# Kernel tuning notes

Measured on AMD Instinct MI355X. Metric: run time of the kernel, lower is better.

The kernel has to match this reference:

```python
import jax, jax.numpy as jnp
import numpy as np
import math

B, T, D = 4, 2048, 1024
N, D_OUT = 1024, 1024
EPS_A = 1e-4
PROJ_BOUND = 1.0


def setup_inputs() -> dict:
    key = jax.random.key(0)
    ks = jax.random.split(key, 4)
    # reset_parameters: rho=0.99, delta0=1.0
    rho, delta0 = 0.99, 1.0
    alpha0 = -math.log(rho) / delta0
    alpha_log_val = math.log(math.expm1(alpha0))
    delta_bias_val = math.log(math.expm1(delta0))
    return {
        "u": jax.random.normal(ks[0], (B, T, D), dtype=jnp.float32),
        "z0": jnp.zeros((B, N), dtype=jnp.float32),
        "W_in_raw": 0.02 * jax.random.normal(ks[1], (N, D), dtype=jnp.float32),
        "W_out_raw": 0.02 * jax.random.normal(ks[2], (D_OUT, N), dtype=jnp.float32),
        "pn_w": 0.02 * jax.random.normal(ks[3], (3 * N, D), dtype=jnp.float32),
        "pn_b": jnp.zeros((3 * N,), dtype=jnp.float32),
        "alpha_log": jnp.full((N,), alpha_log_val, dtype=jnp.float32),
        "delta_bias": jnp.full((N,), delta_bias_val, dtype=jnp.float32),
        "log_gamma": jnp.float32(0.0),
    }


def _bounded_linear(x, W, bound):
    # y = x @ (W/scale)^T with ||W/scale||_2 <= bound (exact spectral norm)
    sigma = jnp.maximum(jnp.linalg.norm(W, ord=2), 1e-5)
    scale = jnp.maximum(sigma / bound, 1.0)
    return x @ (W / scale).T


def reference(u, z0, W_in_raw, W_out_raw, pn_w, pn_b, alpha_log, delta_bias, log_gamma):
    g = jnp.exp(log_gamma)
    u_scaled = g * _bounded_linear(u, W_in_raw, PROJ_BOUND)        # (B,T,N)
    raw = u @ pn_w.T + pn_b                                        # (B,T,3N)
    delta_raw, b_raw, c_raw = jnp.split(raw, 3, axis=-1)
    delta = jax.nn.softplus(delta_raw + delta_bias)
    alpha = jax.nn.softplus(alpha_log)                             # (N,)
    a = jnp.minimum(jnp.exp(-delta * alpha), 1.0 - EPS_A)          # (B,T,N)
    b = jnp.tanh(b_raw)
    c = jnp.tanh(c_raw)
    # exact spectral norm of [[a,b],[c,0]] per coordinate
    p = a * a + c * c
    r = b * b
    q = a * b
    disc = (p - r) * (p - r) + 4.0 * q * q
    lam_max = 0.5 * (p + r + jnp.sqrt(disc + 1e-12))
    sigma = jnp.sqrt(lam_max + 1e-12)
    scale = jnp.maximum(sigma, 1.0)
    a, b, c = a / scale, b / scale, c / scale
    # diagonal recurrence z_{t+1} = a_t * z_t + b_t * u_scaled_t via associative scan
    bu = b * u_scaled
    bu = bu.at[:, 0].add(a[:, 0] * z0)
    def combine(x, y):
        a1, b1 = x
        a2, b2 = y
        return (a2 * a1, a2 * b1 + b2)
    _, z_next = jax.lax.associative_scan(combine, (a, bu), axis=1)  # z_1..z_T (B,T,N)
    # y_t = W_out (c_t * z_t) with z_t = state BEFORE update (one-step delay)
    states = jnp.concatenate([z0[:, None, :], z_next[:, :-1, :]], axis=1)  # z_0..z_{T-1}
    y_hat = c * states
    y = _bounded_linear(y_hat, W_out_raw, PROJ_BOUND)              # (B,T,D_out)
    return y
```

## Files before the change

### kernel.cpp

```cpp
#include <hip/hip_runtime.h>
#include <stdint.h>

#define B_ 4
#define T_ 2048
#define D_ 1024
#define N_ 1024
#define TC 16
#define NCH (T_/TC)
#define SQN 6

typedef __attribute__((ext_vector_type(4))) float f32x4;
typedef __attribute__((ext_vector_type(8))) short bf16x8;
typedef __attribute__((ext_vector_type(4))) unsigned short us4;

__device__ __forceinline__ unsigned short f2bf(float f){
  unsigned int u = __float_as_uint(f);
  return (unsigned short)((u + 0x7fffu + ((u >> 16) & 1u)) >> 16);
}
__device__ __forceinline__ float bf2f(unsigned short h){
  return __uint_as_float(((unsigned int)h) << 16);
}

__device__ __forceinline__ float inv_scale(const float* __restrict__ sc, int z){
  float ll = 0.f, w = 1.f, t = 1.f;
  #pragma unroll
  for (int i = 0; i <= SQN; i++){
    t = sc[8 + 2*i + z];
    ll += w * __logf(t);
    w *= 0.5f;
  }
  float F = sc[8 + 2*(SQN+1) + z];
  ll += w * __logf(F / (t*t));
  float sig = fmaxf(__expf(0.5f * ll), 1e-5f);
  return 1.f / fmaxf(sig, 1.f);
}

__device__ __forceinline__ float softplusf(float x){
  return (x > 0.f) ? (x + __logf(1.f + __expf(-x))) : __logf(1.f + __expf(x));
}
__device__ __forceinline__ float tanhfastf(float x){
  float e = __expf(2.f * x);
  return 1.f - 2.f/(e + 1.f);
}
__device__ __forceinline__ void abc_from(float pin, float draw, float braw, float craw,
    float alpha, float ginv, float& a_o, float& bu_o, float& c_o){
  float sp = softplusf(draw);
  float av = __expf(-sp * alpha);
  av = fminf(av, 1.f - 1e-4f);
  float bv = tanhfastf(braw);
  float cv = tanhfastf(craw);
  float p = av*av + cv*cv;
  float r = bv*bv;
  float q = av*bv;
  float pr = p - r;
  float disc = pr*pr + 4.f*q*q;
  float lam = 0.5f*(p + r + sqrtf(disc + 1e-12f));
  float inv = fminf(rsqrtf(lam + 1e-12f), 1.f);
  a_o = av * inv;
  c_o = cv * inv;
  bu_o = (bv * inv) * (pin * ginv);
}

#define U4    2097152
#define WIN4   262144
#define PNW4   786432
#define WOUT4  262144
#define CONV_BLOCKS ((U4 + WIN4 + PNW4 + WOUT4 + 255)/256)

__global__ void k_convert_all(const float* __restrict__ u, const float* __restrict__ Win,
                              const float* __restrict__ pnw, const float* __restrict__ Wout,
                              unsigned short* __restrict__ u16, unsigned short* __restrict__ Wcat16,
                              unsigned short* __restrict__ Wout16, float* __restrict__ sc){
  if (blockIdx.x == 0 && threadIdx.x < 64) sc[threadIdx.x] = 0.f;
  long i = (long)blockIdx.x * 256 + threadIdx.x;
  const float* src; long o; size_t didx; unsigned short* dbuf;
  if (i < U4){
    src = u; o = i; dbuf = u16; didx = (size_t)o;
  } else if (i < U4+WIN4){
    o = i - U4; src = Win;
    int n = (int)(o >> 8), c4 = (int)(o & 255);
    dbuf = Wcat16; didx = (size_t)(4*n)*256 + c4;
  } else if (i < U4+WIN4+PNW4){
    o = i - (U4+WIN4); src = pnw;
    int m = (int)(o >> 8), c4 = (int)(o & 255);
    int s = (m >> 10) + 1, n = m & 1023;
    dbuf = Wcat16; didx = (size_t)(4*n + s)*256 + c4;
  } else if (i < U4+WIN4+PNW4+WOUT4){
    o = i - (U4+WIN4+PNW4); src = Wout; dbuf = Wout16; didx = (size_t)o;
  } else return;
  float4 v = ((const float4*)src)[o];
  us4 w;
  w.x = f2bf(v.x); w.y = f2bf(v.y); w.z = f2bf(v.z); w.w = f2bf(v.w);
  ((us4*)dbuf)[didx] = w;
}

__device__ __forceinline__ void load_lds16(const unsigned short* g, unsigned short* l){
  __builtin_amdgcn_global_load_lds((const __attribute__((address_space(1))) void*)g,
                                   (__attribute__((address_space(3))) void*)l, 16, 0, 0);
}

__global__ __launch_bounds__(256) void k_pgemm(
    const unsigned short* __restrict__ A,
    const unsigned short* __restrict__ Bmat,
    const float* __restrict__ alog, const float* __restrict__ dbias,
    const float* __restrict__ pnb, const float* __restrict__ lgam,
    const float* __restrict__ sc,
    unsigned int* __restrict__ G1,
    float* __restrict__ G2,
    float* __restrict__ Asum, float* __restrict__ Ssum)
{
  __shared__ alignas(16) unsigned short As[128*64];
  __shared__ alignas(16) unsigned short Bs[128*64];
  const int tid = threadIdx.x;
  const int wid = tid >> 6;
  const int lane = tid & 63;
  const int bn = blockIdx.x, bm = blockIdx.y;
  const int K = 1024;

  const int wr = wid >> 1, wc = wid & 1;
  const int rg = lane >> 3;
  const int cby = (lane & 7) << 4;
  const int srow0 = wid * 32;
  const int frow = lane & 15;
  const int kgrp = lane >> 4;

  const unsigned short* ap[4];
  const unsigned short* bp[4];
  unsigned short* adst[4];
  unsigned short* bdst[4];
  #pragma unroll
  for (int i = 0; i < 4; i++){
    int r = srow0 + i*8 + rg;
    int cb = cby ^ ((r & 7) << 4);
    ap[i] = A    + (size_t)(bm*128 + r)*K + (cb >> 1);
    bp[i] = Bmat + (size_t)(bn*128 + r)*K + (cb >> 1);
    adst[i] = As + (srow0 + i*8)*64;
    bdst[i] = Bs + (srow0 + i*8)*64;
  }
  int aoff[4][2], boff[4][2];
  #pragma unroll
  for (int m = 0; m < 4; m++){
    int r = wr*64 + m*16 + frow;
    #pragma unroll
    for (int kk = 0; kk < 2; kk++)
      aoff[m][kk] = r*128 + ((kk*64 + kgrp*16) ^ ((r & 7) << 4));
  }
  #pragma unroll
  for (int n2 = 0; n2 < 4; n2++){
    int r = wc*64 + n2*16 + frow;
    #pragma unroll
    for (int kk = 0; kk < 2; kk++)
      boff[n2][kk] = r*128 + ((kk*64 + kgrp*16) ^ ((r & 7) << 4));
  }

  f32x4 acc[4][4] = {};

  for (int kt = 0; kt < K; kt += 64){
    #pragma unroll
    for (int i = 0; i < 4; i++){
      load_lds16(ap[i], adst[i]);
      load_lds16(bp[i], bdst[i]);
      ap[i] += 64; bp[i] += 64;
    }
    __syncthreads();
    #pragma unroll
    for (int kk = 0; kk < 2; kk++){
      bf16x8 af[4], bfv[4];
      #pragma unroll
      for (int m = 0; m < 4; m++)
        af[m] = *(const bf16x8*)((const char*)As + aoff[m][kk]);
      #pragma unroll
      for (int n2 = 0; n2 < 4; n2++)
        bfv[n2] = *(const bf16x8*)((const char*)Bs + boff[n2][kk]);
      #pragma unroll
      for (int m = 0; m < 4; m++)
        #pragma unroll
        for (int n2 = 0; n2 < 4; n2++)
          acc[m][n2] = __builtin_amdgcn_mfma_f32_16x16x32_bf16(af[m], bfv[n2], acc[m][n2], 0, 0, 0);
    }
    __syncthreads();
  }

  const int q = (lane >> 2) & 3;
  const int s = lane & 3;
  const bool sb0 = (lane & 1) != 0;
  const bool sb1 = (lane & 2) != 0;
  const float ginv = __expf(lgam[0]) * inv_scale(sc, 0);

  float alpP[4], bdP[4], bbP[4], bcP[4];
  #pragma unroll
  for (int n2 = 0; n2 < 4; n2++){
    int n = bn*32 + wc*16 + n2*4 + q;
    alpP[n2] = softplusf(alog[n]);
    bdP[n2] = dbias[n] + pnb[n];
    bbP[n2] = pnb[N_ + n];
    bcP[n2] = pnb[2*N_ + n];
  }

  #pragma unroll
  for (int m = 0; m < 4; m++){
    #pragma unroll
    for (int n2 = 0; n2 < 4; n2++){
      f32x4 v = acc[m][n2];
      { float x = sb0 ? v[0] : v[1]; float y = __shfl_xor(x, 1, 64); if (sb0) v[0] = y; else v[1] = y; }
      { float x = sb0 ? v[2] : v[3]; float y = __shfl_xor(x, 1, 64); if (sb0) v[2] = y; else v[3] = y; }
      { float x = sb1 ? v[0] : v[2]; float y = __shfl_xor(x, 2, 64); if (sb1) v[0] = y; else v[2] = y; }
      { float x = sb1 ? v[1] : v[3]; float y = __shfl_xor(x, 2, 64); if (sb1) v[1] = y; else v[3] = y; }
      float a, bu, c;
      abc_from(v[0], v[1] + bdP[n2], v[2] + bbP[n2], v[3] + bcP[n2], alpP[n2], ginv, a, bu, c);
      const int row = bm*128 + wr*64 + m*16 + kgrp*4 + s;
      const int n = bn*32 + wc*16 + n2*4 + q;
      G1[(size_t)row*N_ + n] = (unsigned int)f2bf(a) | ((unsigned int)f2bf(c) << 16);
      G2[(size_t)row*N_ + n] = bu;
      float Ar = a, Sr = bu;
      { float Ap = __shfl_xor(Ar,1,64), Sp = __shfl_xor(Sr,1,64);
        if (lane & 1){ Sr = fmaf(Ar, Sp, Sr); } else { Sr = fmaf(Ap, Sr, Sp); } Ar *= Ap; }
      { float Ap = __shfl_xor(Ar,2,64), Sp = __shfl_xor(Sr,2,64);
        if (lane & 2){ Sr = fmaf(Ar, Sp, Sr); } else { Sr = fmaf(Ap, Sr, Sp); } Ar *= Ap; }
      { float Ap = __shfl_xor(Ar,16,64), Sp = __shfl_xor(Sr,16,64);
        if (lane & 16){ Sr = fmaf(Ar, Sp, Sr); } else { Sr = fmaf(Ap, Sr, Sp); } Ar *= Ap; }
      { float Ap = __shfl_xor(Ar,32,64), Sp = __shfl_xor(Sr,32,64);
        if (lane & 32){ Sr = fmaf(Ar, Sp, Sr); } else { Sr = fmaf(Ap, Sr, Sp); } Ar *= Ap; }
      if ((lane & 0x33) == 0){
        const size_t ci = (size_t)(row >> 4)*N_ + n;
        Asum[ci] = Ar; Ssum[ci] = Sr;
      }
    }
  }
}

__global__ __launch_bounds__(256) void k_gemm(
    const unsigned short* __restrict__ A,
    const unsigned short* __restrict__ Bmat,
    float* __restrict__ C,
    int M, int N, int K,
    const float* __restrict__ sc, int step)
{
  __shared__ alignas(16) unsigned short As[128*64];
  __shared__ alignas(16) unsigned short Bs[128*64];
  const int tid = threadIdx.x;
  const int wid = tid >> 6;
  const int lane = tid & 63;
  const int bn = blockIdx.x, bm = blockIdx.y;

  float outscale = (step >= 0) ? inv_scale(sc, step) : 1.f;

  const int wr = wid >> 1, wc = wid & 1;
  const int rg = lane >> 3;
  const int cby = (lane & 7) << 4;
  const int srow0 = wid * 32;
  const int frow = lane & 15;
  const int kgrp = lane >> 4;

  const unsigned short* ap[4];
  const unsigned short* bp[4];
  unsigned short* adst[4];
  unsigned short* bdst[4];
  #pragma unroll
  for (int i = 0; i < 4; i++){
    int r = srow0 + i*8 + rg;
    int cb = cby ^ ((r & 7) << 4);
    ap[i] = A    + (size_t)(bm*128 + r)*K + (cb >> 1);
    bp[i] = Bmat + (size_t)(bn*128 + r)*K + (cb >> 1);
    adst[i] = As + (srow0 + i*8)*64;
    bdst[i] = Bs + (srow0 + i*8)*64;
  }
  int aoff[4][2], boff[4][2];
  #pragma unroll
  for (int m = 0; m < 4; m++){
    int r = wr*64 + m*16 + frow;
    #pragma unroll
    for (int kk = 0; kk < 2; kk++)
      aoff[m][kk] = r*128 + ((kk*64 + kgrp*16) ^ ((r & 7) << 4));
  }
  #pragma unroll
  for (int n2 = 0; n2 < 4; n2++){
    int r = wc*64 + n2*16 + frow;
    #pragma unroll
    for (int kk = 0; kk < 2; kk++)
      boff[n2][kk] = r*128 + ((kk*64 + kgrp*16) ^ ((r & 7) << 4));
  }

  f32x4 acc[4][4] = {};

  for (int kt = 0; kt < K; kt += 64){
    #pragma unroll
    for (int i = 0; i < 4; i++){
      load_lds16(ap[i], adst[i]);
      load_lds16(bp[i], bdst[i]);
      ap[i] += 64; bp[i] += 64;
    }
    __syncthreads();
    #pragma unroll
    for (int kk = 0; kk < 2; kk++){
      bf16x8 af[4], bfv[4];
      #pragma unroll
      for (int m = 0; m < 4; m++)
        af[m] = *(const bf16x8*)((const char*)As + aoff[m][kk]);
      #pragma unroll
      for (int n2 = 0; n2 < 4; n2++)
        bfv[n2] = *(const bf16x8*)((const char*)Bs + boff[n2][kk]);
      #pragma unroll
      for (int m = 0; m < 4; m++)
        #pragma unroll
        for (int n2 = 0; n2 < 4; n2++)
          acc[m][n2] = __builtin_amdgcn_mfma_f32_16x16x32_bf16(af[m], bfv[n2], acc[m][n2], 0, 0, 0);
    }
    __syncthreads();
  }

  const int row0 = bm*128 + wr*64;
  const int col0 = bn*128 + wc*64 + frow;
  #pragma unroll
  for (int m = 0; m < 4; m++){
    #pragma unroll
    for (int n2 = 0; n2 < 4; n2++){
      const int col = col0 + n2*16;
      const int rb = row0 + m*16 + kgrp*4;
      #pragma unroll
      for (int j = 0; j < 4; j++)
        C[(size_t)(rb + j)*N + col] = acc[m][n2][j] * outscale;
    }
  }
}

__global__ __launch_bounds__(256) void k_sq(
    const unsigned short* __restrict__ A0, unsigned short* __restrict__ C0,
    const unsigned short* __restrict__ A1, unsigned short* __restrict__ C1,
    float* __restrict__ sc, int step)
{
  __shared__ alignas(16) unsigned short As0[64*128], Bs0[64*128];
  __shared__ alignas(16) unsigned short As1[64*128], Bs1[64*128];
  const int tid = threadIdx.x;
  const int wid = tid >> 6;
  const int lane = tid & 63;
  const int z = blockIdx.z;

  int x = blockIdx.x, bm = 0;
  while (x >= 16 - bm){ x -= 16 - bm; bm++; }
  const int bn = bm + x;

  const unsigned short* A = z ? A1 : A0;
  unsigned short* C = z ? C1 : C0;
  const size_t rs = (step == 0 && z == 0) ? 4096 : 1024;
  float outscale = 1.f;
  if (step > 0){ float t = sc[8 + (step-1)*2 + z]; outscale = 1.f/(t*t); }

  const int wr = wid >> 1, wc = wid & 1;
  const int frow = lane & 15;
  const int kgrp = lane >> 4;

  const int srl = lane >> 4;
  const int sgr = lane & 15;
  const int swzr = wid*4 + srl;
  const int scol_e = ((sgr ^ swzr) << 3);

  const size_t Arow = (size_t)bm * 64;
  const size_t Brow = (size_t)bn * 64;

  f32x4 acc[2][2] = {};

  auto stage = [&](unsigned short* as, unsigned short* bs, int t){
    const int kt = t * 128;
    #pragma unroll
    for (int i = 0; i < 4; i++){
      int r = i*16 + wid*4 + srl;
      load_lds16(A + (Arow + r)*rs + kt + scol_e, as + (i*16 + wid*4)*128);
      load_lds16(A + (Brow + r)*rs + kt + scol_e, bs + (i*16 + wid*4)*128);
    }
  };

  auto compute = [&](const unsigned short* as, const unsigned short* bs){
    #pragma unroll
    for (int ks = 0; ks < 4; ks++){
      const int kb = ks*64 + kgrp*16;
      bf16x8 af[2], bfv[2];
      #pragma unroll
      for (int m = 0; m < 2; m++){
        int r = wr*32 + m*16 + frow;
        af[m] = *(const bf16x8*)((const char*)as + r*256 + (kb ^ (frow << 4)));
      }
      #pragma unroll
      for (int n2 = 0; n2 < 2; n2++){
        int r = wc*32 + n2*16 + frow;
        bfv[n2] = *(const bf16x8*)((const char*)bs + r*256 + (kb ^ (frow << 4)));
      }
      #pragma unroll
      for (int m = 0; m < 2; m++)
        #pragma unroll
        for (int n2 = 0; n2 < 2; n2++)
          acc[m][n2] = __builtin_amdgcn_mfma_f32_16x16x32_bf16(af[m], bfv[n2], acc[m][n2], 0, 0, 0);
    }
  };

  stage(As0, Bs0, 0);
  __syncthreads();
  for (int t2 = 0; t2 < 8; t2 += 2){
    if (t2 + 1 < 8) stage(As1, Bs1, t2 + 1);
    compute(As0, Bs0);
    __syncthreads();
    if (t2 + 2 < 8) stage(As0, Bs0, t2 + 2);
    compute(As1, Bs1);
    __syncthreads();
  }

  const int row0 = bm*64 + wr*32;
  const int col0 = bn*64 + wc*32 + frow;
  float fr = 0.f;
  #pragma unroll
  for (int m = 0; m < 2; m++){
    #pragma unroll
    for (int n2 = 0; n2 < 2; n2++){
      const int col = col0 + n2*16;
      const int rb = row0 + m*16 + kgrp*4;
      us4 tw;
      #pragma unroll
      for (int j = 0; j < 4; j++){
        float v = acc[m][n2][j] * outscale;
        unsigned short h = f2bf(v);
        C[(size_t)(rb + j)*1024 + col] = h;
        tw[j] = h;
        fr += v*v;
      }
      if (bm != bn)
        *(us4*)(C + (size_t)col*1024 + rb) = tw;
    }
  }
  if (bm == bn && wr == wc){
    int j = frow - kgrp*4;
    if (j >= 0 && j < 4){
      float d = (acc[0][0][j] + acc[1][1][j]) * outscale;
      atomicAdd(&sc[8 + step*2 + z], d);
    }
  }
  if (step == SQN){
    if (bm != bn) fr *= 2.f;
    #pragma unroll
    for (int off = 32; off; off >>= 1) fr += __shfl_down(fr, off, 64);
    if (lane == 0) atomicAdd(&sc[8 + 2*(SQN+1) + z], fr);
  }
}

__global__ __launch_bounds__(256) void k_scan(
    const unsigned int* __restrict__ G1, const float* __restrict__ G2,
    const float* __restrict__ Asum, const float* __restrict__ Ssum,
    const float* __restrict__ z0, unsigned short* __restrict__ yh)
{
  const int tid = threadIdx.x;
  const int n0 = tid*4;
  const int ch = blockIdx.x, b = blockIdx.y;
  float z[4];
  #pragma unroll
  for (int j = 0; j < 4; j++) z[j] = z0[b*N_ + n0 + j];
  for (int c2 = 0; c2 < ch; c2++){
    const size_t idx = (size_t)(b*NCH + c2)*N_ + n0;
    float4 Av = *(const float4*)(Asum + idx);
    float4 Sv = *(const float4*)(Ssum + idx);
    z[0] = fmaf(Av.x, z[0], Sv.x);
    z[1] = fmaf(Av.y, z[1], Sv.y);
    z[2] = fmaf(Av.z, z[2], Sv.z);
    z[3] = fmaf(Av.w, z[3], Sv.w);
  }
  const size_t base = (size_t)(b*T_ + ch*TC)*N_ + n0;
  const unsigned int* g1 = G1 + base;
  const float* g2 = G2 + base;
  unsigned short* Y = yh + base;
  #pragma unroll 4
  for (int i = 0; i < TC; i++){
    uint4 pac = *(const uint4*)g1;
    float4 bu = *(const float4*)g2;
    us4 ow;
    #pragma unroll
    for (int j = 0; j < 4; j++){
      unsigned int p = j==0 ? pac.x : j==1 ? pac.y : j==2 ? pac.z : pac.w;
      float buj     = j==0 ? bu.x  : j==1 ? bu.y  : j==2 ? bu.z  : bu.w;
      float a = bf2f((unsigned short)(p & 0xffffu));
      float c = bf2f((unsigned short)(p >> 16));
      float yv = c * z[j];
      z[j] = fmaf(a, z[j], buj);
      ow[j] = f2bf(yv);
    }
    *(us4*)Y = ow;
    g1 += N_; g2 += N_; Y += N_;
  }
}

extern "C" void kernel_launch(void* const* d_in, const int* in_sizes, int n_in,
                              void* d_out, int out_size, void* d_ws, size_t ws_size,
                              hipStream_t stream)
{
  const float* u    = (const float*)d_in[0];
  const float* z0   = (const float*)d_in[1];
  const float* Win  = (const float*)d_in[2];
  const float* Wout = (const float*)d_in[3];
  const float* pnw  = (const float*)d_in[4];
  const float* pnb  = (const float*)d_in[5];
  const float* alog = (const float*)d_in[6];
  const float* dbias= (const float*)d_in[7];
  const float* lgam = (const float*)d_in[8];

  char* ws = (char*)d_ws;
  size_t off = 0;
  auto alloc = [&](size_t bytes) -> void* {
    void* p = ws + off;
    off += (bytes + 255) & ~(size_t)255;
    return p;
  };
  float*          sc     = (float*)         alloc(1024);
  unsigned short* u16    = (unsigned short*)alloc((size_t)8192*1024*2);
  unsigned short* Wcat16 = (unsigned short*)alloc((size_t)4096*1024*2);
  unsigned short* Wout16 = (unsigned short*)alloc((size_t)1024*1024*2);
  unsigned int*   G1     = (unsigned int*)  alloc((size_t)8192*1024*4);
  float*          G2     = (float*)         alloc((size_t)8192*1024*4);
  unsigned short* yh16   = (unsigned short*)alloc((size_t)8192*1024*2);
  unsigned short* Hping  = (unsigned short*)alloc((size_t)2*1024*1024*2);
  unsigned short* Hpong  = (unsigned short*)alloc((size_t)2*1024*1024*2);
  float*          Asum   = (float*)alloc((size_t)B_*NCH*N_*4);
  float*          Ssum   = (float*)alloc((size_t)B_*NCH*N_*4);

  k_convert_all<<<CONV_BLOCKS, 256, 0, stream>>>(u, Win, pnw, Wout, u16, Wcat16, Wout16, sc);

  dim3 gsq(136, 1, 2);
  k_sq<<<gsq, 256, 0, stream>>>(Wcat16, Hping, Wout16, Hping + (size_t)1024*1024, sc, 0);
  unsigned short* hin = Hping;
  unsigned short* hout = Hpong;
  for (int s = 1; s <= SQN; s++){
    k_sq<<<gsq, 256, 0, stream>>>(hin, hout, hin + (size_t)1024*1024, hout + (size_t)1024*1024, sc, s);
    unsigned short* t = hin; hin = hout; hout = t;
  }

  dim3 g1(4096/128, 8192/128);
  k_pgemm<<<g1, 256, 0, stream>>>(u16, Wcat16, alog, dbias, pnb, lgam, sc, G1, G2, Asum, Ssum);

  dim3 gsc(NCH, B_);
  k_scan<<<gsc, 256, 0, stream>>>(G1, G2, Asum, Ssum, z0, yh16);

  dim3 g2(1024/128, 8192/128);
  k_gemm<<<g2, 256, 0, stream>>>(yh16, Wout16, d_out == nullptr ? nullptr : (float*)d_out,
                                 8192, 1024, 1024, sc, 1);
}
```

Baseline: 290.3 us.

## Move chunk-scan reduction out of projection GEMM epilogue into separate kernel

The projection GEMM epilogue no longer does lane shuffles to transpose accumulators or computes per-chunk scan summaries. Swapping the MFMA operand order puts each lane's four values (input, delta, b, c) for one coordinate in one accumulator register group. A new k_scanA kernel rereads G1/G2 to compute per-chunk products and sums before the existing scan pass. This cuts shuffle and epilogue cost in the GEMM but adds a kernel launch and an extra read of the gate buffers. k_gemm also gains an unused template option for bf16 output.

```diff
diff --git a/kernel.cpp b/kernel.cpp
--- a/kernel.cpp
+++ b/kernel.cpp
@@ -41,24 +41,6 @@
 __device__ __forceinline__ float tanhfastf(float x){
   float e = __expf(2.f * x);
   return 1.f - 2.f/(e + 1.f);
-}
-__device__ __forceinline__ void abc_from(float pin, float draw, float braw, float craw,
-    float alpha, float ginv, float& a_o, float& bu_o, float& c_o){
-  float sp = softplusf(draw);
-  float av = __expf(-sp * alpha);
-  av = fminf(av, 1.f - 1e-4f);
-  float bv = tanhfastf(braw);
-  float cv = tanhfastf(craw);
-  float p = av*av + cv*cv;
-  float r = bv*bv;
-  float q = av*bv;
-  float pr = p - r;
-  float disc = pr*pr + 4.f*q*q;
-  float lam = 0.5f*(p + r + sqrtf(disc + 1e-12f));
-  float inv = fminf(rsqrtf(lam + 1e-12f), 1.f);
-  a_o = av * inv;
-  c_o = cv * inv;
-  bu_o = (bv * inv) * (pin * ginv);
 }
 
 #define U4    2097152
@@ -106,8 +88,7 @@
     const float* __restrict__ pnb, const float* __restrict__ lgam,
     const float* __restrict__ sc,
     unsigned int* __restrict__ G1,
-    float* __restrict__ G2,
-    float* __restrict__ Asum, float* __restrict__ Ssum)
+    float* __restrict__ G2)
 {
   __shared__ alignas(16) unsigned short As[128*64];
   __shared__ alignas(16) unsigned short Bs[128*64];
@@ -176,63 +157,54 @@
       for (int m = 0; m < 4; m++)
         #pragma unroll
         for (int n2 = 0; n2 < 4; n2++)
-          acc[m][n2] = __builtin_amdgcn_mfma_f32_16x16x32_bf16(af[m], bfv[n2], acc[m][n2], 0, 0, 0);
+          acc[m][n2] = __builtin_amdgcn_mfma_f32_16x16x32_bf16(bfv[n2], af[m], acc[m][n2], 0, 0, 0);
     }
     __syncthreads();
   }
 
-  const int q = (lane >> 2) & 3;
-  const int s = lane & 3;
-  const bool sb0 = (lane & 1) != 0;
-  const bool sb1 = (lane & 2) != 0;
   const float ginv = __expf(lgam[0]) * inv_scale(sc, 0);
-
-  float alpP[4], bdP[4], bbP[4], bcP[4];
-  #pragma unroll
-  for (int n2 = 0; n2 < 4; n2++){
-    int n = bn*32 + wc*16 + n2*4 + q;
-    alpP[n2] = softplusf(alog[n]);
-    bdP[n2] = dbias[n] + pnb[n];
-    bbP[n2] = pnb[N_ + n];
-    bcP[n2] = pnb[2*N_ + n];
-  }
-
-  #pragma unroll
-  for (int m = 0; m < 4; m++){
-    #pragma unroll
-    for (int n2 = 0; n2 < 4; n2++){
-      f32x4 v = acc[m][n2];
-      { float x = sb0 ? v[0] : v[1]; float y = __shfl_xor(x, 1, 64); if (sb0) v[0] = y; else v[1] = y; }
-      { float x = sb0 ? v[2] : v[3]; float y = __shfl_xor(x, 1, 64); if (sb0) v[2] = y; else v[3] = y; }
-      { float x = sb1 ? v[0] : v[2]; float y = __shfl_xor(x, 2, 64); if (sb1) v[0] = y; else v[2] = y; }
-      { float x = sb1 ? v[1] : v[3]; float y = __shfl_xor(x, 2, 64); if (sb1) v[1] = y; else v[3] = y; }
-      float a, bu, c;
-      abc_from(v[0], v[1] + bdP[n2], v[2] + bbP[n2], v[3] + bcP[n2], alpP[n2], ginv, a, bu, c);
-      const int row = bm*128 + wr*64 + m*16 + kgrp*4 + s;
-      const int n = bn*32 + wc*16 + n2*4 + q;
-      G1[(size_t)row*N_ + n] = (unsigned int)f2bf(a) | ((unsigned int)f2bf(c) << 16);
-      G2[(size_t)row*N_ + n] = bu;
-      float Ar = a, Sr = bu;
-      { float Ap = __shfl_xor(Ar,1,64), Sp = __shfl_xor(Sr,1,64);
-        if (lane & 1){ Sr = fmaf(Ar, Sp, Sr); } else { Sr = fmaf(Ap, Sr, Sp); } Ar *= Ap; }
-      { float Ap = __shfl_xor(Ar,2,64), Sp = __shfl_xor(Sr,2,64);
-        if (lane & 2){ Sr = fmaf(Ar, Sp, Sr); } else { Sr = fmaf(Ap, Sr, Sp); } Ar *= Ap; }
-      { float Ap = __shfl_xor(Ar,16,64), Sp = __shfl_xor(Sr,16,64);
-        if (lane & 16){ Sr = fmaf(Ar, Sp, Sr); } else { Sr = fmaf(Ap, Sr, Sp); } Ar *= Ap; }
-      { float Ap = __shfl_xor(Ar,32,64), Sp = __shfl_xor(Sr,32,64);
-        if (lane & 32){ Sr = fmaf(Ar, Sp, Sr); } else { Sr = fmaf(Ap, Sr, Sp); } Ar *= Ap; }
-      if ((lane & 0x33) == 0){
-        const size_t ci = (size_t)(row >> 4)*N_ + n;
-        Asum[ci] = Ar; Ssum[ci] = Sr;
-      }
-    }
-  }
-}
-
+  float alpha[4], bd[4], bb[4], bc[4];
+  #pragma unroll
+  for (int nw = 0; nw < 4; nw++){
+    int n = bn*32 + wc*16 + nw*4 + kgrp;
+    alpha[nw] = softplusf(alog[n]);
+    bd[nw] = dbias[n] + pnb[n];
+    bb[nw] = pnb[N_ + n];
+    bc[nw] = pnb[2*N_ + n];
+  }
+  const int t0 = bm*128 + wr*64 + frow;
+  #pragma unroll
+  for (int mu = 0; mu < 4; mu++){
+    const size_t rowb = (size_t)(t0 + mu*16) * N_;
+    #pragma unroll
+    for (int nw = 0; nw < 4; nw++){
+      const int n = bn*32 + wc*16 + nw*4 + kgrp;
+      f32x4 v = acc[mu][nw];
+      float lp = __logf(1.f + __expf(v[1] + bd[nw]));
+      float av = fminf(__expf(-alpha[nw]*lp), 1.f - 1e-4f);
+      float bv = tanhfastf(v[2] + bb[nw]);
+      float cv = tanhfastf(v[3] + bc[nw]);
+      float p = av*av + cv*cv;
+      float r = bv*bv;
+      float q = av*bv;
+      float pr = p - r;
+      float disc = pr*pr + 4.f*q*q;
+      float lam = 0.5f*(p + r + sqrtf(disc + 1e-12f));
+      float inv = fminf(rsqrtf(lam + 1e-12f), 1.f);
+      float a = av * inv;
+      float c = cv * inv;
+      float bu = (bv * inv) * (v[0] * ginv);
+      G1[rowb + n] = (unsigned int)f2bf(a) | ((unsigned int)f2bf(c) << 16);
+      G2[rowb + n] = bu;
+    }
+  }
+}
+
+template<int OUTBF16>
 __global__ __launch_bounds__(256) void k_gemm(
     const unsigned short* __restrict__ A,
     const unsigned short* __restrict__ Bmat,
-    float* __restrict__ C,
+    void* __restrict__ C0,
     int M, int N, int K,
     const float* __restrict__ sc, int step)
 {
@@ -243,6 +215,7 @@
   const int lane = tid & 63;
   const int bn = blockIdx.x, bm = blockIdx.y;
 
+  char* C = (char*)C0;
   float outscale = (step >= 0) ? inv_scale(sc, step) : 1.f;
 
   const int wr = wid >> 1, wc = wid & 1;
@@ -318,8 +291,11 @@
       const int col = col0 + n2*16;
       const int rb = row0 + m*16 + kgrp*4;
       #pragma unroll
-      for (int j = 0; j < 4; j++)
-        C[(size_t)(rb + j)*N + col] = acc[m][n2][j] * outscale;
+      for (int j = 0; j < 4; j++){
+        float v = acc[m][n2][j] * outscale;
+        if (OUTBF16) ((unsigned short*)C)[(size_t)(rb + j)*N + col] = f2bf(v);
+        else         ((float*)C)[(size_t)(rb + j)*N + col] = v;
+      }
     }
   }
 }
@@ -441,7 +417,35 @@
   }
 }
 
-__global__ __launch_bounds__(256) void k_scan(
+__global__ __launch_bounds__(256) void k_scanA(
+    const unsigned int* __restrict__ G1, const float* __restrict__ G2,
+    float* __restrict__ Asum, float* __restrict__ Ssum)
+{
+  const int tid = threadIdx.x;
+  const int n0 = blockIdx.y*512 + tid*2;
+  const int ch = blockIdx.x, b = blockIdx.z;
+  const size_t base = (size_t)(b*T_ + ch*TC)*N_ + n0;
+
+  uint2 g1[TC]; float2 g2[TC];
+  #pragma unroll
+  for (int i = 0; i < TC; i++){
+    g1[i] = *(const uint2*)(G1 + base + (size_t)i*N_);
+    g2[i] = *(const float2*)(G2 + base + (size_t)i*N_);
+  }
+  float A0 = 1.f, A1 = 1.f, S0 = 0.f, S1 = 0.f;
+  #pragma unroll
+  for (int i = 0; i < TC; i++){
+    float a0 = bf2f((unsigned short)(g1[i].x & 0xffffu));
+    float a1 = bf2f((unsigned short)(g1[i].y & 0xffffu));
+    S0 = fmaf(a0, S0, g2[i].x); A0 *= a0;
+    S1 = fmaf(a1, S1, g2[i].y); A1 *= a1;
+  }
+  const size_t idx = (size_t)(b*NCH + ch)*N_ + n0;
+  *(float2*)(Asum + idx) = make_float2(A0, A1);
+  *(float2*)(Ssum + idx) = make_float2(S0, S1);
+}
+
+__global__ __launch_bounds__(256) void k_scanB(
     const unsigned int* __restrict__ G1, const float* __restrict__ G2,
     const float* __restrict__ Asum, const float* __restrict__ Ssum,
     const float* __restrict__ z0, unsigned short* __restrict__ yh)
@@ -530,12 +534,13 @@
   }
 
   dim3 g1(4096/128, 8192/128);
-  k_pgemm<<<g1, 256, 0, stream>>>(u16, Wcat16, alog, dbias, pnb, lgam, sc, G1, G2, Asum, Ssum);
-
-  dim3 gsc(NCH, B_);
-  k_scan<<<gsc, 256, 0, stream>>>(G1, G2, Asum, Ssum, z0, yh16);
+  k_pgemm<<<g1, 256, 0, stream>>>(u16, Wcat16, alog, dbias, pnb, lgam, sc, G1, G2);
+
+  dim3 ga(NCH, 2, B_);
+  k_scanA<<<ga, 256, 0, stream>>>(G1, G2, Asum, Ssum);
+  dim3 gb(NCH, B_);
+  k_scanB<<<gb, 256, 0, stream>>>(G1, G2, Asum, Ssum, z0, yh16);
 
   dim3 g2(1024/128, 8192/128);
-  k_gemm<<<g2, 256, 0, stream>>>(yh16, Wout16, d_out == nullptr ? nullptr : (float*)d_out,
-                                 8192, 1024, 1024, sc, 1);
-}
+  k_gemm<0><<<g2, 256, 0, stream>>>(yh16, Wout16, d_out, 8192, 1024, 1024, sc, 1);
+}
```

After: 283.9 us. 2.2% less time.
